# Kernel tuning notes

Measured on AMD Instinct MI355X. Metric: run time of the kernel, lower is better.

The kernel has to match this reference:

```python
import jax, jax.numpy as jnp
import numpy as np
import math

B, S, CZ, H, CH = 1, 384, 128, 4, 32


def setup_inputs() -> dict:
    key = jax.random.key(0)
    ks = jax.random.split(key, 12)
    sd = 0.02
    return {
        "z": jax.random.normal(ks[0], (B, S, S, CZ), dtype=jnp.float32),
        "ln_w": jnp.ones((CZ,), dtype=jnp.float32),
        "ln_b": jnp.zeros((CZ,), dtype=jnp.float32),
        "Wq": jax.random.normal(ks[1], (H * CH, CZ), dtype=jnp.float32) * sd,
        "Wk": jax.random.normal(ks[2], (CH, CZ), dtype=jnp.float32) * sd,
        "Wv": jax.random.normal(ks[3], (CH, CZ), dtype=jnp.float32) * sd,
        "Wb": jax.random.normal(ks[4], (H, CZ), dtype=jnp.float32) * sd,
        "Wg": jax.random.normal(ks[5], (H * CH, CZ), dtype=jnp.float32) * sd,
        "bg": jnp.zeros((H * CH,), dtype=jnp.float32),
        "Wo": jax.random.normal(ks[6], (CZ, H * CH), dtype=jnp.float32) * sd,
        "bo": jnp.zeros((CZ,), dtype=jnp.float32),
    }


def reference(z, ln_w, ln_b, Wq, Wk, Wv, Wb, Wg, bg, Wo, bo):
    b_, s_, _, cz = z.shape
    h = Wb.shape[0]          # n_heads
    ch = Wk.shape[0]         # c_hidden
    # LayerNorm over c_z (eps = 1e-5, torch default)
    mu = jnp.mean(z, axis=-1, keepdims=True)
    var = jnp.mean(jnp.square(z - mu), axis=-1, keepdims=True)
    zn = (z - mu) * jax.lax.rsqrt(var + 1e-5) * ln_w + ln_b
    # projections (starting=True: attend along rows i over key index k)
    q = (zn @ Wq.T).reshape(b_, s_, s_, h, ch)   # [B,I,J,H,C]
    k = zn @ Wk.T                                 # [B,I,K,C] shared across heads
    v = zn @ Wv.T                                 # [B,I,K,C]
    bias = zn @ Wb.T                              # [B,I,J,H]
    g = jax.nn.sigmoid(zn @ Wg.T + bg)            # [B,I,J,H*C]
    scale = 1.0 / math.sqrt(ch)
    logits = jnp.einsum('bijhc,bikc->bihjk', q, k) * scale  # [B,I,H,J,K]
    # NOTE: faithful to source — bias broadcasts along the KEY axis (softmax-invariant)
    logits = logits + jnp.transpose(bias, (0, 1, 3, 2))[..., None]
    w = jax.nn.softmax(logits, axis=-1)           # [B,I,H,J,K]
    o = jnp.einsum('bihjk,bikc->bijhc', w, v).reshape(b_, s_, s_, h * ch)
    o = g * o
    return o @ Wo.T + bo
```

## Files before the change

kernel.cpp:

```cpp
#include <hip/hip_runtime.h>
#include <math.h>


typedef unsigned short u16;
typedef __attribute__((ext_vector_type(8))) short short8;
typedef __attribute__((ext_vector_type(4))) short short4v;
typedef __attribute__((ext_vector_type(4))) float float4v;

union U8 { short8 s; u16 h[8]; };
union U4 { short4v s; u16 h[4]; };

__device__ __forceinline__ float bf2f(u16 x){
    unsigned v = ((unsigned)x) << 16;
    float f; __builtin_memcpy(&f, &v, 4);
    return f;
}
__device__ __forceinline__ u16 f2bf(float f){
    unsigned v; __builtin_memcpy(&v, &f, 4);
    unsigned r = (v + 0x7FFFu + ((v >> 16) & 1u)) >> 16;
    return (u16)r;
}
__device__ __forceinline__ float exp2_fast(float x){
    float r; asm("v_exp_f32 %0, %1" : "=v"(r) : "v"(x));
    return r;
}
__device__ __forceinline__ short8 pack8f_s(const float* p, float s){
    const float4 a = ((const float4*)p)[0];
    const float4 b = ((const float4*)p)[1];
    U8 u;
    u.h[0]=f2bf(a.x*s); u.h[1]=f2bf(a.y*s); u.h[2]=f2bf(a.z*s); u.h[3]=f2bf(a.w*s);
    u.h[4]=f2bf(b.x*s); u.h[5]=f2bf(b.y*s); u.h[6]=f2bf(b.z*s); u.h[7]=f2bf(b.w*s);
    return u.s;
}

__global__ __launch_bounds__(256) void k0a_wconv(
    const float* __restrict__ Wq, const float* __restrict__ Wk,
    const float* __restrict__ Wv, const float* __restrict__ Wg,
    u16* __restrict__ Wbf)
{
    const int i = blockIdx.x * 256 + threadIdx.x;
    const int e = i * 8;
    const int n = e >> 7, c0 = e & 127;
    const float* src; float s = 1.f;
    if (n < 128)      { src = Wq + n*128 + c0; s = 0.17677669529663689f * 1.4426950408889634f; }
    else if (n < 160) { src = Wk + (n-128)*128 + c0; }
    else if (n < 192) { src = Wv + (n-160)*128 + c0; }
    else              { src = Wg + (n-192)*128 + c0; }
    *(short8*)(Wbf + e) = pack8f_s(src, s);
}

__global__ __launch_bounds__(256) void k0b_wconv(
    const float* __restrict__ Wo, u16* __restrict__ WoBf)
{
    const int e = (blockIdx.x * 256 + threadIdx.x) * 8;
    *(short8*)(WoBf + e) = pack8f_s(Wo + e, 1.f);
}

__global__ __launch_bounds__(256, 2) void k1_ln_proj(
    const float* __restrict__ z, const float* __restrict__ lnw, const float* __restrict__ lnb,
    const u16* __restrict__ Wbf, const float* __restrict__ bg,
    u16* __restrict__ Qbuf, u16* __restrict__ KVbuf, u16* __restrict__ Gbuf)
{
    __shared__ __align__(16) u16 zn[64][136];
    const int tid = threadIdx.x;
    const long rowg0 = (long)blockIdx.x * 64;

    {
        const int r = tid >> 2, p = tid & 3;
        const float* src = z + (rowg0 + r) * 128 + p * 32;
        float x[32];
        #pragma unroll
        for (int q = 0; q < 8; q++){
            const float4 v = ((const float4*)src)[q];
            x[q*4+0]=v.x; x[q*4+1]=v.y; x[q*4+2]=v.z; x[q*4+3]=v.w;
        }
        float s = 0.f, ss = 0.f;
        #pragma unroll
        for (int t = 0; t < 32; t++){ s += x[t]; ss += x[t]*x[t]; }
        s += __shfl_xor(s, 1);  ss += __shfl_xor(ss, 1);
        s += __shfl_xor(s, 2);  ss += __shfl_xor(ss, 2);
        const float mean = s * (1.f/128.f);
        const float var  = ss * (1.f/128.f) - mean*mean;
        const float rstd = rsqrtf(var + 1e-5f);
        #pragma unroll
        for (int t = 0; t < 32; t++){
            const int c = p*32 + t;
            zn[r][c] = f2bf((x[t]-mean)*rstd*lnw[c] + lnb[c]);
        }
    }
    __syncthreads();

    const int lane = tid & 63, wave = tid >> 6;
    const int l15 = lane & 15, quad = lane >> 4;

    short8 ZN[4][4];
    #pragma unroll
    for (int m = 0; m < 4; m++)
        #pragma unroll
        for (int ks = 0; ks < 4; ks++)
            ZN[m][ks] = *(const short8*)&zn[m*16 + l15][ks*32 + quad*8];

    #pragma unroll
    for (int g = 0; g < 5; g++){
        const int nt = wave*5 + g;
        const u16* wp = Wbf + (nt*16 + l15)*128 + quad*8;
        short8 WF[4];
        #pragma unroll
        for (int ks = 0; ks < 4; ks++) WF[ks] = *(const short8*)(wp + ks*32);
        const int n0 = nt*16 + quad*4;
        #pragma unroll
        for (int m = 0; m < 4; m++){
            float4v c = {0.f,0.f,0.f,0.f};
            #pragma unroll
            for (int ks = 0; ks < 4; ks++)
                c = __builtin_amdgcn_mfma_f32_16x16x32_bf16(WF[ks], ZN[m][ks], c, 0, 0, 0);
            const long row = rowg0 + m*16 + l15;
            if (nt < 8){
                U4 u;
                #pragma unroll
                for (int r = 0; r < 4; r++) u.h[r] = f2bf(c[r]);
                *(short4v*)(Qbuf + row*128 + n0) = u.s;
            } else if (nt < 10){
                U4 u;
                #pragma unroll
                for (int r = 0; r < 4; r++) u.h[r] = f2bf(c[r]);
                *(short4v*)(KVbuf + row*64 + (n0 - 128)) = u.s;
            } else if (nt < 12){
                U4 u;
                #pragma unroll
                for (int r = 0; r < 4; r++) u.h[r] = f2bf(c[r]);
                *(short4v*)(KVbuf + row*64 + (n0 - 160) + 32) = u.s;
            } else {
                const float4 b4 = *(const float4*)&bg[n0 - 192];
                U4 u;
                u.h[0] = f2bf(1.f/(1.f + __expf(-(c[0] + b4.x))));
                u.h[1] = f2bf(1.f/(1.f + __expf(-(c[1] + b4.y))));
                u.h[2] = f2bf(1.f/(1.f + __expf(-(c[2] + b4.z))));
                u.h[3] = f2bf(1.f/(1.f + __expf(-(c[3] + b4.w))));
                *(short4v*)(Gbuf + row*128 + (n0 - 192)) = u.s;
            }
        }
    }
}

__global__ __launch_bounds__(512, 4) void k2_attn(
    const u16* __restrict__ KVbuf, const u16* __restrict__ Gbuf, u16* __restrict__ QObuf)
{
    __shared__ __align__(16) u16 Ks[384][40];
    __shared__ __align__(16) u16 Vt[32][392];
    __shared__ __align__(16) u16 Pb[8][16][72];
    const int i = blockIdx.x >> 1, jh = blockIdx.x & 1;
    const int tid = threadIdx.x;
    const u16* kvsrc = KVbuf + (long)i * 384 * 64;
    {
        for (int idx = tid; idx < 384*8; idx += 512){
            const int k = idx >> 3, c8 = idx & 7;
            U8 d; d.s = *(const short8*)(kvsrc + k*64 + c8*8);
            if (c8 < 4) *(short8*)&Ks[k][c8*8] = d.s;
            else {
                const int c0 = (c8 - 4) * 8;
                #pragma unroll
                for (int jj = 0; jj < 8; jj++) Vt[c0 + jj][k] = d.h[jj];
            }
        }
    }
    __syncthreads();

    const int lane = tid & 63, wave = tid >> 6;
    const int l15 = lane & 15, quad = lane >> 4;
    const int h = wave >> 1, sub = wave & 1;
    const u16* qbase = QObuf + (long)i * 384 * 128 + h * 32;
    const u16* gbase = Gbuf  + (long)i * 384 * 128 + h * 32;
    u16* obase = QObuf + (long)i * 384 * 128 + h * 32;

    for (int t = 0; t < 6; t++){
        const int j0 = (jh*12 + sub*6 + t) * 16;
        const short8 aq = *(const short8*)(qbase + (long)(j0 + l15)*128 + quad*8);
        float4v acc[24];
        #pragma unroll
        for (int kt = 0; kt < 24; kt++){
            const short8 bk = *(const short8*)&Ks[kt*16 + l15][quad*8];
            float4v zero = {0.f,0.f,0.f,0.f};
            acc[kt] = __builtin_amdgcn_mfma_f32_16x16x32_bf16(aq, bk, zero, 0, 0, 0);
        }
        float inv[4];
        #pragma unroll
        for (int r = 0; r < 4; r++){
            float mx = -1e30f;
            #pragma unroll
            for (int kt = 0; kt < 24; kt++) mx = fmaxf(mx, acc[kt][r]);
            mx = fmaxf(mx, __shfl_xor(mx, 1));
            mx = fmaxf(mx, __shfl_xor(mx, 2));
            mx = fmaxf(mx, __shfl_xor(mx, 4));
            mx = fmaxf(mx, __shfl_xor(mx, 8));
            float sum = 0.f;
            #pragma unroll
            for (int kt = 0; kt < 24; kt++){ acc[kt][r] = exp2_fast(acc[kt][r] - mx); sum += acc[kt][r]; }
            sum += __shfl_xor(sum, 1);
            sum += __shfl_xor(sum, 2);
            sum += __shfl_xor(sum, 4);
            sum += __shfl_xor(sum, 8);
            inv[r] = 1.f / sum;
        }
        float4v oacc[2] = {{0.f,0.f,0.f,0.f},{0.f,0.f,0.f,0.f}};
        #pragma unroll
        for (int cc = 0; cc < 6; cc++){
            #pragma unroll
            for (int j = 0; j < 4; j++){
                const int kt = cc*4 + j;
                #pragma unroll
                for (int r = 0; r < 4; r++)
                    Pb[wave][quad*4 + r][j*16 + l15] = f2bf(acc[kt][r]);
            }
            #pragma unroll
            for (int kj = 0; kj < 2; kj++){
                const int kk = cc*2 + kj;
                const short8 ap = *(const short8*)&Pb[wave][l15][kj*32 + quad*8];
                #pragma unroll
                for (int ct = 0; ct < 2; ct++){
                    const short8 bv = *(const short8*)&Vt[ct*16 + l15][kk*32 + quad*8];
                    oacc[ct] = __builtin_amdgcn_mfma_f32_16x16x32_bf16(ap, bv, oacc[ct], 0, 0, 0);
                }
            }
        }
        #pragma unroll
        for (int ct = 0; ct < 2; ct++){
            const int c = ct*16 + l15;
            #pragma unroll
            for (int r = 0; r < 4; r++){
                const int row = j0 + quad*4 + r;
                const float gv = bf2f(gbase[(long)row*128 + c]);
                obase[(long)row*128 + c] = f2bf(gv * (oacc[ct][r] * inv[r]));
            }
        }
    }
}

__global__ __launch_bounds__(256, 2) void k3_outproj(
    const u16* __restrict__ Obuf, const u16* __restrict__ WoBf, const float* __restrict__ bo,
    float* __restrict__ out)
{
    const int tid = threadIdx.x, lane = tid & 63, wave = tid >> 6;
    const int l15 = lane & 15, quad = lane >> 4;
    short8 WF[2][4];
    float4 b4[2];
    #pragma unroll
    for (int g = 0; g < 2; g++){
        const u16* wp = WoBf + ((wave*2 + g)*16 + l15)*128 + quad*8;
        #pragma unroll
        for (int ks = 0; ks < 4; ks++) WF[g][ks] = *(const short8*)(wp + ks*32);
        b4[g] = *(const float4*)&bo[(wave*2 + g)*16 + quad*4];
    }
    #pragma unroll
    for (int slab = 0; slab < 2; slab++){
        const long row0 = ((long)blockIdx.x * 2 + slab) * 64;
        #pragma unroll
        for (int m = 0; m < 4; m++){
            short8 OF[4];
            const u16* ap = Obuf + (row0 + m*16 + l15)*128 + quad*8;
            #pragma unroll
            for (int ks = 0; ks < 4; ks++) OF[ks] = *(const short8*)(ap + ks*32);
            #pragma unroll
            for (int g = 0; g < 2; g++){
                float4v c = {0.f,0.f,0.f,0.f};
                #pragma unroll
                for (int ks = 0; ks < 4; ks++)
                    c = __builtin_amdgcn_mfma_f32_16x16x32_bf16(WF[g][ks], OF[ks], c, 0, 0, 0);
                const int n0 = (wave*2 + g)*16 + quad*4;
                const long row = row0 + m*16 + l15;
                float4 o4;
                o4.x = c[0] + b4[g].x; o4.y = c[1] + b4[g].y;
                o4.z = c[2] + b4[g].z; o4.w = c[3] + b4[g].w;
                *(float4*)(out + row*128 + n0) = o4;
            }
        }
    }
}

extern "C" void kernel_launch(void* const* d_in, const int* in_sizes, int n_in,
                              void* d_out, int out_size, void* d_ws, size_t ws_size,
                              hipStream_t stream)
{
    (void)in_sizes; (void)n_in; (void)out_size; (void)ws_size;
    const float* z   = (const float*)d_in[0];
    const float* lnw = (const float*)d_in[1];
    const float* lnb = (const float*)d_in[2];
    const float* Wq  = (const float*)d_in[3];
    const float* Wk  = (const float*)d_in[4];
    const float* Wv  = (const float*)d_in[5];
    const float* Wg  = (const float*)d_in[7];
    const float* bg  = (const float*)d_in[8];
    const float* Wo  = (const float*)d_in[9];
    const float* bo  = (const float*)d_in[10];

    u16* Qbuf = (u16*)d_ws;
    u16* KV   = Qbuf + 147456L*128;
    u16* Gbuf = (u16*)d_out;
    u16* Wbf  = Gbuf + 147456L*128;
    u16* WoBf = KV;

    k0a_wconv<<<dim3(20), dim3(256), 0, stream>>>(Wq, Wk, Wv, Wg, Wbf);
    k1_ln_proj<<<dim3(2304), dim3(256), 0, stream>>>(z, lnw, lnb, Wbf, bg,
                                                     Qbuf, KV, Gbuf);
    k2_attn<<<dim3(768), dim3(512), 0, stream>>>(KV, Gbuf, Qbuf);
    k0b_wconv<<<dim3(8), dim3(256), 0, stream>>>(Wo, WoBf);
    k3_outproj<<<dim3(1152), dim3(256), 0, stream>>>(Qbuf, WoBf, bo, (float*)d_out);
}
```

Baseline: 326.1 us.

## Fuse output projection into attention kernel when workspace allows

Adds a fused attention kernel that, after each block has written its gated attention output for 192 rows, runs the Wo projection on those rows and writes the fp32 output directly. This removes the separate out-projection launch and one global read pass. Gbuf moves from the output buffer to workspace so the fused kernel can write the output safely. The fused path depends on the workspace being large enough, and falls back to the old path otherwise. It also relies on a threadfence plus syncthreads to make the block's own global writes visible before rereading them.

```diff
diff --git a/kernel.cpp b/kernel.cpp
--- a/kernel.cpp
+++ b/kernel.cpp
@@ -143,95 +143,130 @@
     }
 }
 
+#define K2_BODY(DO_FUSED)                                                          \
+    __shared__ __align__(16) u16 Ks[384][40];                                      \
+    __shared__ __align__(16) u16 Vt[32][392];                                      \
+    __shared__ __align__(16) u16 Pb[8][16][72];                                    \
+    const int i = blockIdx.x >> 1, jh = blockIdx.x & 1;                            \
+    const int tid = threadIdx.x;                                                   \
+    const u16* kvsrc = KVbuf + (long)i * 384 * 64;                                 \
+    {                                                                              \
+        for (int idx = tid; idx < 384*8; idx += 512){                              \
+            const int k = idx >> 3, c8 = idx & 7;                                  \
+            U8 d; d.s = *(const short8*)(kvsrc + k*64 + c8*8);                     \
+            if (c8 < 4) *(short8*)&Ks[k][c8*8] = d.s;                              \
+            else {                                                                 \
+                const int c0 = (c8 - 4) * 8;                                       \
+                _Pragma("unroll")                                                  \
+                for (int jj = 0; jj < 8; jj++) Vt[c0 + jj][k] = d.h[jj];           \
+            }                                                                      \
+        }                                                                          \
+    }                                                                              \
+    __syncthreads();                                                               \
+    const int lane = tid & 63, wave = tid >> 6;                                    \
+    const int l15 = lane & 15, quad = lane >> 4;                                   \
+    const int h = wave >> 1, sub = wave & 1;                                       \
+    const u16* qbase = QObuf + (long)i * 384 * 128 + h * 32;                       \
+    const u16* gbase = Gbuf  + (long)i * 384 * 128 + h * 32;                       \
+    u16* obase = QObuf + (long)i * 384 * 128 + h * 32;                             \
+    for (int t = 0; t < 6; t++){                                                   \
+        const int j0 = (jh*12 + sub*6 + t) * 16;                                   \
+        const short8 aq = *(const short8*)(qbase + (long)(j0 + l15)*128 + quad*8); \
+        float4v acc[24];                                                           \
+        _Pragma("unroll")                                                          \
+        for (int kt = 0; kt < 24; kt++){                                           \
+            const short8 bk = *(const short8*)&Ks[kt*16 + l15][quad*8];            \
+            float4v zero = {0.f,0.f,0.f,0.f};                                      \
+            acc[kt] = __builtin_amdgcn_mfma_f32_16x16x32_bf16(aq, bk, zero, 0,0,0);\
+        }                                                                          \
+        float inv[4];                                                              \
+        _Pragma("unroll")                                                          \
+        for (int r = 0; r < 4; r++){                                               \
+            float mx = -1e30f;                                                     \
+            _Pragma("unroll")                                                      \
+            for (int kt = 0; kt < 24; kt++) mx = fmaxf(mx, acc[kt][r]);            \
+            mx = fmaxf(mx, __shfl_xor(mx, 1));                                     \
+            mx = fmaxf(mx, __shfl_xor(mx, 2));                                     \
+            mx = fmaxf(mx, __shfl_xor(mx, 4));                                     \
+            mx = fmaxf(mx, __shfl_xor(mx, 8));                                     \
+            float sum = 0.f;                                                       \
+            _Pragma("unroll")                                                      \
+            for (int kt = 0; kt < 24; kt++){                                       \
+                acc[kt][r] = exp2_fast(acc[kt][r] - mx); sum += acc[kt][r]; }      \
+            sum += __shfl_xor(sum, 1);                                             \
+            sum += __shfl_xor(sum, 2);                                             \
+            sum += __shfl_xor(sum, 4);                                             \
+            sum += __shfl_xor(sum, 8);                                             \
+            inv[r] = 1.f / sum;                                                    \
+        }                                                                          \
+        float4v oacc[2] = {{0.f,0.f,0.f,0.f},{0.f,0.f,0.f,0.f}};                   \
+        _Pragma("unroll")                                                          \
+        for (int cc = 0; cc < 6; cc++){                                            \
+            _Pragma("unroll")                                                      \
+            for (int j = 0; j < 4; j++){                                           \
+                const int kt = cc*4 + j;                                           \
+                _Pragma("unroll")                                                  \
+                for (int r = 0; r < 4; r++)                                        \
+                    Pb[wave][quad*4 + r][j*16 + l15] = f2bf(acc[kt][r]);           \
+            }                                                                      \
+            _Pragma("unroll")                                                      \
+            for (int kj = 0; kj < 2; kj++){                                        \
+                const int kk = cc*2 + kj;                                          \
+                const short8 ap = *(const short8*)&Pb[wave][l15][kj*32 + quad*8];  \
+                _Pragma("unroll")                                                  \
+                for (int ct = 0; ct < 2; ct++){                                    \
+                    const short8 bv = *(const short8*)&Vt[ct*16 + l15][kk*32 + quad*8]; \
+                    oacc[ct] = __builtin_amdgcn_mfma_f32_16x16x32_bf16(ap, bv, oacc[ct], 0,0,0); \
+                }                                                                  \
+            }                                                                      \
+        }                                                                          \
+        _Pragma("unroll")                                                          \
+        for (int ct = 0; ct < 2; ct++){                                            \
+            const int c = ct*16 + l15;                                             \
+            _Pragma("unroll")                                                      \
+            for (int r = 0; r < 4; r++){                                           \
+                const int row = j0 + quad*4 + r;                                   \
+                const float gv = bf2f(gbase[(long)row*128 + c]);                   \
+                obase[(long)row*128 + c] = f2bf(gv * (oacc[ct][r] * inv[r]));      \
+            }                                                                      \
+        }                                                                          \
+    }
+
 __global__ __launch_bounds__(512, 4) void k2_attn(
     const u16* __restrict__ KVbuf, const u16* __restrict__ Gbuf, u16* __restrict__ QObuf)
 {
-    __shared__ __align__(16) u16 Ks[384][40];
-    __shared__ __align__(16) u16 Vt[32][392];
-    __shared__ __align__(16) u16 Pb[8][16][72];
-    const int i = blockIdx.x >> 1, jh = blockIdx.x & 1;
-    const int tid = threadIdx.x;
-    const u16* kvsrc = KVbuf + (long)i * 384 * 64;
+    K2_BODY(0)
+}
+
+__global__ __launch_bounds__(512, 4) void k2_attn_fused(
+    const u16* __restrict__ KVbuf, const u16* __restrict__ Gbuf, u16* __restrict__ QObuf,
+    const u16* __restrict__ WoBf, const float* __restrict__ bo, float* __restrict__ outp)
+{
+    K2_BODY(1)
+    __threadfence();
+    __syncthreads();
     {
-        for (int idx = tid; idx < 384*8; idx += 512){
-            const int k = idx >> 3, c8 = idx & 7;
-            U8 d; d.s = *(const short8*)(kvsrc + k*64 + c8*8);
-            if (c8 < 4) *(short8*)&Ks[k][c8*8] = d.s;
-            else {
-                const int c0 = (c8 - 4) * 8;
-                #pragma unroll
-                for (int jj = 0; jj < 8; jj++) Vt[c0 + jj][k] = d.h[jj];
-            }
-        }
-    }
-    __syncthreads();
-
-    const int lane = tid & 63, wave = tid >> 6;
-    const int l15 = lane & 15, quad = lane >> 4;
-    const int h = wave >> 1, sub = wave & 1;
-    const u16* qbase = QObuf + (long)i * 384 * 128 + h * 32;
-    const u16* gbase = Gbuf  + (long)i * 384 * 128 + h * 32;
-    u16* obase = QObuf + (long)i * 384 * 128 + h * 32;
-
-    for (int t = 0; t < 6; t++){
-        const int j0 = (jh*12 + sub*6 + t) * 16;
-        const short8 aq = *(const short8*)(qbase + (long)(j0 + l15)*128 + quad*8);
-        float4v acc[24];
-        #pragma unroll
-        for (int kt = 0; kt < 24; kt++){
-            const short8 bk = *(const short8*)&Ks[kt*16 + l15][quad*8];
-            float4v zero = {0.f,0.f,0.f,0.f};
-            acc[kt] = __builtin_amdgcn_mfma_f32_16x16x32_bf16(aq, bk, zero, 0, 0, 0);
-        }
-        float inv[4];
-        #pragma unroll
-        for (int r = 0; r < 4; r++){
-            float mx = -1e30f;
-            #pragma unroll
-            for (int kt = 0; kt < 24; kt++) mx = fmaxf(mx, acc[kt][r]);
-            mx = fmaxf(mx, __shfl_xor(mx, 1));
-            mx = fmaxf(mx, __shfl_xor(mx, 2));
-            mx = fmaxf(mx, __shfl_xor(mx, 4));
-            mx = fmaxf(mx, __shfl_xor(mx, 8));
-            float sum = 0.f;
-            #pragma unroll
-            for (int kt = 0; kt < 24; kt++){ acc[kt][r] = exp2_fast(acc[kt][r] - mx); sum += acc[kt][r]; }
-            sum += __shfl_xor(sum, 1);
-            sum += __shfl_xor(sum, 2);
-            sum += __shfl_xor(sum, 4);
-            sum += __shfl_xor(sum, 8);
-            inv[r] = 1.f / sum;
-        }
-        float4v oacc[2] = {{0.f,0.f,0.f,0.f},{0.f,0.f,0.f,0.f}};
-        #pragma unroll
-        for (int cc = 0; cc < 6; cc++){
-            #pragma unroll
-            for (int j = 0; j < 4; j++){
-                const int kt = cc*4 + j;
-                #pragma unroll
-                for (int r = 0; r < 4; r++)
-                    Pb[wave][quad*4 + r][j*16 + l15] = f2bf(acc[kt][r]);
-            }
-            #pragma unroll
-            for (int kj = 0; kj < 2; kj++){
-                const int kk = cc*2 + kj;
-                const short8 ap = *(const short8*)&Pb[wave][l15][kj*32 + quad*8];
-                #pragma unroll
-                for (int ct = 0; ct < 2; ct++){
-                    const short8 bv = *(const short8*)&Vt[ct*16 + l15][kk*32 + quad*8];
-                    oacc[ct] = __builtin_amdgcn_mfma_f32_16x16x32_bf16(ap, bv, oacc[ct], 0, 0, 0);
-                }
-            }
-        }
-        #pragma unroll
-        for (int ct = 0; ct < 2; ct++){
-            const int c = ct*16 + l15;
-            #pragma unroll
-            for (int r = 0; r < 4; r++){
-                const int row = j0 + quad*4 + r;
-                const float gv = bf2f(gbase[(long)row*128 + c]);
-                obase[(long)row*128 + c] = f2bf(gv * (oacc[ct][r] * inv[r]));
-            }
+        const long rbase = (long)i * 384 + jh * 192;
+        const u16* wp = WoBf + (wave*16 + l15)*128 + quad*8;
+        short8 WF[4];
+        #pragma unroll
+        for (int ks = 0; ks < 4; ks++) WF[ks] = *(const short8*)(wp + ks*32);
+        const int n0 = wave*16 + quad*4;
+        const float4 b4 = *(const float4*)&bo[n0];
+        for (int rt = 0; rt < 12; rt++){
+            short8 OF[4];
+            const u16* ap = QObuf + (rbase + rt*16 + l15)*128 + quad*8;
+            #pragma unroll
+            for (int ks = 0; ks < 4; ks++) OF[ks] = *(const short8*)(ap + ks*32);
+            float4v c = {0.f,0.f,0.f,0.f};
+            #pragma unroll
+            for (int ks = 0; ks < 4; ks++)
+                c = __builtin_amdgcn_mfma_f32_16x16x32_bf16(WF[ks], OF[ks], c, 0, 0, 0);
+            const long row = rbase + rt*16 + l15;
+            float4 o4;
+            o4.x = c[0] + b4.x; o4.y = c[1] + b4.y;
+            o4.z = c[2] + b4.z; o4.w = c[3] + b4.w;
+            *(float4*)(outp + row*128 + n0) = o4;
         }
     }
 }
@@ -281,7 +316,7 @@
                               void* d_out, int out_size, void* d_ws, size_t ws_size,
                               hipStream_t stream)
 {
-    (void)in_sizes; (void)n_in; (void)out_size; (void)ws_size;
+    (void)in_sizes; (void)n_in; (void)out_size;
     const float* z   = (const float*)d_in[0];
     const float* lnw = (const float*)d_in[1];
     const float* lnb = (const float*)d_in[2];
@@ -293,16 +328,34 @@
     const float* Wo  = (const float*)d_in[9];
     const float* bo  = (const float*)d_in[10];
 
-    u16* Qbuf = (u16*)d_ws;
-    u16* KV   = Qbuf + 147456L*128;
-    u16* Gbuf = (u16*)d_out;
-    u16* Wbf  = Gbuf + 147456L*128;
-    u16* WoBf = KV;
-
-    k0a_wconv<<<dim3(20), dim3(256), 0, stream>>>(Wq, Wk, Wv, Wg, Wbf);
-    k1_ln_proj<<<dim3(2304), dim3(256), 0, stream>>>(z, lnw, lnb, Wbf, bg,
-                                                     Qbuf, KV, Gbuf);
-    k2_attn<<<dim3(768), dim3(512), 0, stream>>>(KV, Gbuf, Qbuf);
-    k0b_wconv<<<dim3(8), dim3(256), 0, stream>>>(Wo, WoBf);
-    k3_outproj<<<dim3(1152), dim3(256), 0, stream>>>(Qbuf, WoBf, bo, (float*)d_out);
-}
+    const long NQ = 147456L*128;
+    const long NK = 147456L*64;
+
+    const size_t WS_FUSED = (size_t)(NQ*2 + NK*2 + NQ*2) + 32768 + 81920;
+
+    if (ws_size >= WS_FUSED){
+        u16* Qbuf = (u16*)d_ws;
+        u16* KV   = Qbuf + NQ;
+        u16* Gbuf = KV + NK;
+        u16* WoBf = Gbuf + NQ;
+        u16* Wbf  = WoBf + 16384;
+        k0a_wconv<<<dim3(20), dim3(256), 0, stream>>>(Wq, Wk, Wv, Wg, Wbf);
+        k0b_wconv<<<dim3(8), dim3(256), 0, stream>>>(Wo, WoBf);
+        k1_ln_proj<<<dim3(2304), dim3(256), 0, stream>>>(z, lnw, lnb, Wbf, bg,
+                                                         Qbuf, KV, Gbuf);
+        k2_attn_fused<<<dim3(768), dim3(512), 0, stream>>>(KV, Gbuf, Qbuf,
+                                                           WoBf, bo, (float*)d_out);
+    } else {
+        u16* Qbuf = (u16*)d_ws;
+        u16* KV   = Qbuf + NQ;
+        u16* Gbuf = (u16*)d_out;
+        u16* Wbf  = Gbuf + NQ;
+        u16* WoBf = KV;
+        k0a_wconv<<<dim3(20), dim3(256), 0, stream>>>(Wq, Wk, Wv, Wg, Wbf);
+        k1_ln_proj<<<dim3(2304), dim3(256), 0, stream>>>(z, lnw, lnb, Wbf, bg,
+                                                         Qbuf, KV, Gbuf);
+        k2_attn<<<dim3(768), dim3(512), 0, stream>>>(KV, Gbuf, Qbuf);
+        k0b_wconv<<<dim3(8), dim3(256), 0, stream>>>(Wo, WoBf);
+        k3_outproj<<<dim3(1152), dim3(256), 0, stream>>>(Qbuf, WoBf, bo, (float*)d_out);
+    }
+}
```

Result: slower. 515.1 us (+58.0%).
